# Kernel optimization log

Measured on AMD Instinct MI355X. Metric: run time of the kernel, lower is better.

## Reference

```python
import jax, jax.numpy as jnp
import numpy as np

NUM_NODES = 100000
NUM_HYPEREDGES = 100000
NNZ = 1600000
K = 64
LAMBDA_ORTHO = 0.1


def setup_inputs() -> dict:
    key = jax.random.key(0)
    k1, k2, k3 = jax.random.split(key, 3)
    Z = jax.random.normal(k1, (NUM_NODES, K), dtype=jnp.float32)
    hyperedge_index = jax.random.randint(k2, (2, NNZ), 0, NUM_HYPEREDGES, dtype=jnp.int64)
    hyperedge_weight = jax.random.uniform(k3, (NUM_HYPEREDGES,), dtype=jnp.float32)
    return {
        "Z": Z,
        "hyperedge_index": hyperedge_index,
        "num_nodes": NUM_NODES,
        "hyperedge_weight": hyperedge_weight,
    }


def reference(Z, hyperedge_index, num_nodes, hyperedge_weight):
    E = hyperedge_weight.shape[0]  # num_hyperedges (static)
    node_idx = hyperedge_index[0]
    edge_idx = hyperedge_index[1]

    # Node degree Dv = sum of incident hyperedge weights; clamp zeros to 1.
    w_exp = hyperedge_weight[edge_idx]                                  # [nnz]
    Dv = jax.ops.segment_sum(w_exp, node_idx, num_segments=num_nodes)   # [N]
    Dv = jnp.where(Dv == 0, jnp.ones_like(Dv), Dv)
    Y = Z * (Dv ** -0.5)[:, None]                                       # [N, k]

    # Hyperedge cardinality De (clamped) and raw counts n_e.
    ones = jnp.ones_like(edge_idx, dtype=Z.dtype)
    n_e = jax.ops.segment_sum(ones, edge_idx, num_segments=E)           # [E]
    De = jnp.where(n_e == 0, jnp.ones_like(n_e), n_e)

    # Closed form for the per-edge pairwise-distance loop:
    # 0.5 * sum_{i,j in e} |y_i - y_j|^2 = n_e * sum_i |y_i|^2 - |sum_i y_i|^2
    Yg = Y[node_idx]                                                    # [nnz, k]
    sum_e = jax.ops.segment_sum(Yg, edge_idx, num_segments=E)           # [E, k]
    ss_e = jax.ops.segment_sum(jnp.sum(Yg * Yg, axis=-1), edge_idx, num_segments=E)  # [E]
    per_edge = n_e * ss_e - jnp.sum(sum_e * sum_e, axis=-1)             # [E]
    loss = jnp.sum(hyperedge_weight / De * per_edge)

    # Orthogonality penalty: ||Y^T Y - I||_F
    k = Z.shape[1]
    G = Y.T @ Y - jnp.eye(k, dtype=Z.dtype)
    ortho_loss = jnp.sqrt(jnp.sum(G * G))

    return loss + LAMBDA_ORTHO * ortho_loss
```

## Files before the change

### kernel.cpp

```cpp
#include <hip/hip_runtime.h>
#include <math.h>

#define NNODES 100000
#define NEDGES 100000
#define NNZV   1600000
#define KDIM   64
#define LAMBDA 0.1f

#define NB    782
#define BSH   7
#define BMASK 127
#define CAP   3072
#define A0B   256
#define A0T   1024
#define CHUNK 6250
#define YQB   1024
#define GMB   512

#define OFF_DV      0
#define OFF_G       400128
#define OFF_PART    416512
#define OFF_ZN      419840
#define OFF_GC1     423936
#define OFF_GC2     427264
#define OFF_S1      430592
#define OFF_S2      10039808
#define OFF_YQ      19649024
#define OFF_GPART   26049024

#if defined(__has_builtin)
#if __has_builtin(__builtin_amdgcn_cvt_f32_fp8)
#define HAS_CVT_FP8 1
#endif
#if __has_builtin(__builtin_amdgcn_cvt_pk_fp8_f32)
#define HAS_PK_FP8 1
#endif
#endif

__device__ __forceinline__ int load_node(const unsigned* idx, int i, bool i64) {
    return (int)(i64 ? idx[2 * i] : idx[i]);
}
__device__ __forceinline__ int load_edge(const unsigned* idx, int i, bool i64) {
    return (int)(i64 ? idx[2 * (NNZV + i)] : idx[NNZV + i]);
}

__device__ __forceinline__ unsigned char enc_fp8(float x) {
    unsigned u = __float_as_uint(x);
    unsigned s = (u >> 31) << 7;
    unsigned mag = u & 0x7FFFFFFFu;
    if (mag >= 0x43E00000u) return (unsigned char)(s | 0x7Eu);
    if (mag < 0x3C800000u) {
        float a = __uint_as_float(mag);
        int m = (int)rintf(a * 512.0f);
        if (m >= 8) return (unsigned char)(s | 0x08u);
        return (unsigned char)(s | (unsigned)m);
    }
    unsigned lsb = (mag >> 20) & 1u;
    mag += 0x0007FFFFu + lsb;
    unsigned e = (mag >> 23) - 120u;
    return (unsigned char)(s | (e << 3) | ((mag >> 20) & 7u));
}

__device__ __forceinline__ unsigned pack_fp8x4(float y0, float y1, float y2, float y3) {
#ifdef HAS_PK_FP8
    int q = 0;
    q = __builtin_amdgcn_cvt_pk_fp8_f32(y0, y1, q, false);
    q = __builtin_amdgcn_cvt_pk_fp8_f32(y2, y3, q, true);
    return (unsigned)q;
#else
    return (unsigned)enc_fp8(y0) | ((unsigned)enc_fp8(y1) << 8) |
           ((unsigned)enc_fp8(y2) << 16) | ((unsigned)enc_fp8(y3) << 24);
#endif
}

template <int SEL>
__device__ __forceinline__ float dec_fp8(unsigned v) {
#ifdef HAS_CVT_FP8
    return __builtin_amdgcn_cvt_f32_fp8(v, SEL);
#else
    unsigned b = (v >> (8 * SEL)) & 0xFFu;
    unsigned e = (b >> 3) & 15u, m = b & 7u;
    float f = e ? __uint_as_float(((e + 120u) << 23) | (m << 20))
                : (float)m * 0.001953125f;
    return (b & 128u) ? -f : f;
#endif
}

__global__ void init_kernel(unsigned* __restrict__ gcur1, unsigned* __restrict__ gcur2) {
    int b = blockIdx.x * 256 + threadIdx.x;
    if (b < NB) {
        gcur1[b] = (unsigned)b * CAP;
        gcur2[b] = (unsigned)b * CAP;
    }
}

__global__ __launch_bounds__(A0T) void sort_kernel(const unsigned* __restrict__ idx,
                                                   unsigned* __restrict__ gcur1,
                                                   unsigned* __restrict__ gcur2,
                                                   unsigned* __restrict__ S1,
                                                   unsigned* __restrict__ S2) {
    __shared__ unsigned stage[CHUNK];
    __shared__ unsigned lhist[NB], lcur[NB], gbase[NB];
    __shared__ unsigned wsum[16], fred[16];
    int which = blockIdx.x >> 8, chunk = blockIdx.x & (A0B - 1);
    int t = threadIdx.x, wave = t >> 6, lane = t & 63;

    unsigned hv = idx[2 * t + 1];
#pragma unroll
    for (int off = 32; off; off >>= 1) hv |= __shfl_xor(hv, off);
    if (lane == 0) fred[wave] = hv;
    for (int j = t; j < NB; j += A0T) lhist[j] = 0u;
    __syncthreads();
    unsigned o = 0;
#pragma unroll
    for (int k = 0; k < 16; ++k) o |= fred[k];
    bool i64 = (o == 0u);

    int base = chunk * CHUNK;
    if (which == 0) {
        for (int i = base + t; i < base + CHUNK; i += A0T)
            atomicAdd(&lhist[load_edge(idx, i, i64) >> BSH], 1u);
    } else {
        for (int i = base + t; i < base + CHUNK; i += A0T)
            atomicAdd(&lhist[load_node(idx, i, i64) >> BSH], 1u);
    }
    __syncthreads();

    unsigned v = (t < NB) ? lhist[t] : 0u;
    unsigned x = v;
#pragma unroll
    for (int off = 1; off < 64; off <<= 1) {
        unsigned y = __shfl_up(x, off);
        if (lane >= off) x += y;
    }
    if (lane == 63) wsum[wave] = x;
    __syncthreads();
    if (t < 16) {
        unsigned a = wsum[t], y = a;
#pragma unroll
        for (int off = 1; off < 16; off <<= 1) {
            unsigned z = __shfl_up(y, off);
            if (t >= off) y += z;
        }
        wsum[t] = y - a;
    }
    __syncthreads();
    if (t < NB) lcur[t] = wsum[wave] + x - v;
    __syncthreads();

    for (int i = base + t; i < base + CHUNK; i += A0T) {
        int node = load_node(idx, i, i64);
        int edge = load_edge(idx, i, i64);
        unsigned key, val;
        if (which == 0) {
            key = (unsigned)edge >> BSH;
            val = (unsigned)node | ((unsigned)(edge & BMASK) << 17);
        } else {
            key = (unsigned)node >> BSH;
            val = (unsigned)edge | ((unsigned)(node & BMASK) << 17);
        }
        unsigned p = atomicAdd(&lcur[key], 1u);
        stage[p] = val;
    }
    __syncthreads();

    unsigned* gcur = which ? gcur2 : gcur1;
    if (t < NB) {
        unsigned c = lhist[t];
        gbase[t] = c ? atomicAdd(&gcur[t], c) : 0u;
    }
    __syncthreads();

    unsigned* S = which ? S2 : S1;
    int li = lane & 7;
    for (int bb = wave * 8 + (lane >> 3); bb < NB; bb += 128) {
        unsigned c = lhist[bb];
        unsigned st = lcur[bb] - c;
        unsigned g = gbase[bb];
        for (unsigned m = li; m < c; m += 8) S[g + m] = stage[st + m];
    }
}

__global__ __launch_bounds__(256) void dvb_kernel(const unsigned* __restrict__ S2,
                                                  const unsigned* __restrict__ gcur2,
                                                  const float* __restrict__ w,
                                                  float* __restrict__ Dv) {
    __shared__ float acc[128];
    int t = threadIdx.x, b = blockIdx.x;
    if (t < 128) acc[t] = 0.0f;
    __syncthreads();
    unsigned cnt = gcur2[b] - (unsigned)b * CAP;
    const unsigned* src = S2 + (size_t)b * CAP;
    for (unsigned i = t; i < cnt; i += 256) {
        unsigned e = src[i];
        atomicAdd(&acc[e >> 17], w[e & 0x1FFFFu]);
    }
    __syncthreads();
    int node = b * 128 + t;
    if (t < 128 && node < NNODES) Dv[node] = acc[t];
}

__global__ __launch_bounds__(256) void yq_kernel(const float* __restrict__ Z,
                                                 const float* __restrict__ Dv,
                                                 unsigned* __restrict__ Yq32,
                                                 float* __restrict__ ZN) {
    __shared__ float red[256];
    int t = threadIdx.x;
    float zn = 0.0f;
    for (int i4 = blockIdx.x * 256 + t; i4 < NNODES * 16; i4 += YQB * 256) {
        float4 v = ((const float4*)Z)[i4];
        float d = Dv[i4 >> 4];
        bool good = d > 0.0f;
        float r = good ? rsqrtf(d) : 1.0f;
        zn += good ? (v.x * v.x + v.y * v.y + v.z * v.z + v.w * v.w) : 0.0f;
        Yq32[i4] = pack_fp8x4(v.x * r, v.y * r, v.z * r, v.w * r);
    }
    red[t] = zn;
    __syncthreads();
    for (int s = 128; s > 0; s >>= 1) {
        if (t < s) red[t] += red[t + s];
        __syncthreads();
    }
    if (t == 0) ZN[blockIdx.x] = red[0];
}

__global__ __launch_bounds__(256) void gmat_kernel(const unsigned* __restrict__ Yq32,
                                                   float* __restrict__ Gpart) {
    __shared__ float ys[64][KDIM];
    float acc[16];
#pragma unroll
    for (int i = 0; i < 16; ++i) acc[i] = 0.0f;
    int t = threadIdx.x;
    int c = t & 63;
    int r0 = (t >> 6) * 16;
    for (int base = blockIdx.x * 64; base < NNODES; base += GMB * 64) {
        int rows = min(64, NNODES - base);
        __syncthreads();
        for (int j = t; j < rows * 16; j += 256) {
            unsigned v = Yq32[base * 16 + j];
            int row = j >> 4, q4 = (j & 15) * 4;
            ys[row][q4 + 0] = dec_fp8<0>(v);
            ys[row][q4 + 1] = dec_fp8<1>(v);
            ys[row][q4 + 2] = dec_fp8<2>(v);
            ys[row][q4 + 3] = dec_fp8<3>(v);
        }
        __syncthreads();
#pragma unroll 4
        for (int i = 0; i < rows; ++i) {
            float yc = ys[i][c];
#pragma unroll
            for (int rr = 0; rr < 16; ++rr) acc[rr] += ys[i][r0 + rr] * yc;
        }
    }
    float* gp = Gpart + (size_t)blockIdx.x * (KDIM * KDIM);
#pragma unroll
    for (int rr = 0; rr < 16; ++rr) gp[(r0 + rr) * KDIM + c] = acc[rr];
}

__global__ __launch_bounds__(256) void greduce_kernel(const float* __restrict__ Gpart,
                                                      float* __restrict__ G) {
    __shared__ float r[256];
    int t = threadIdx.x;
    int e0 = blockIdx.x * 32;
    int psub = t >> 5, e = e0 + (t & 31);
    float s = 0.0f;
    for (int p = psub; p < GMB; p += 8)
        s += Gpart[(size_t)p * (KDIM * KDIM) + e];
    r[t] = s;
    __syncthreads();
    if (t < 32) {
        float v = r[t];
#pragma unroll
        for (int k = 1; k < 8; ++k) v += r[t + 32 * k];
        G[e0 + t] = v;
    }
}

__global__ __launch_bounds__(512) void bedge_kernel(const unsigned* __restrict__ Yq32,
                                                    const float* __restrict__ w,
                                                    const unsigned* __restrict__ S1,
                                                    const unsigned* __restrict__ gcur1,
                                                    float* __restrict__ part) {
    __shared__ unsigned lhist[128], loffs[128], lcur[128];
    __shared__ unsigned snode[CAP];
    __shared__ float wred[8];
    int t = threadIdx.x, b = blockIdx.x;
    if (t < 128) lhist[t] = 0u;
    __syncthreads();
    unsigned cnt = gcur1[b] - (unsigned)b * CAP;
    const unsigned* src = S1 + (size_t)b * CAP;
    for (unsigned i = t; i < cnt; i += 512)
        atomicAdd(&lhist[src[i] >> 17], 1u);
    __syncthreads();
    if (t < 64) {
        unsigned a = lhist[2 * t], bb = lhist[2 * t + 1];
        unsigned sp = a + bb, x = sp;
#pragma unroll
        for (int off = 1; off < 64; off <<= 1) {
            unsigned y = __shfl_up(x, off);
            if (t >= off) x += y;
        }
        unsigned ex = x - sp;
        loffs[2 * t] = ex;          lcur[2 * t] = ex;
        loffs[2 * t + 1] = ex + a;  lcur[2 * t + 1] = ex + a;
    }
    __syncthreads();
    for (unsigned i = t; i < cnt; i += 512) {
        unsigned e = src[i];
        unsigned pos = atomicAdd(&lcur[e >> 17], 1u);
        snode[pos] = e & 0x1FFFFu;
    }
    __syncthreads();
    int wv = t >> 6, lane = t & 63, ms = lane >> 4, kq = lane & 15;
    float acc = 0.0f;
    for (int el = wv; el < 64; el += 8) {
        int eA = el, eB = el + 64;
        unsigned nA = lhist[eA], nB = lhist[eB];
        if (nA == 0 && nB == 0) continue;
        unsigned begA = loffs[eA], begB = loffs[eB];
        float a0 = 0, a1 = 0, a2 = 0, a3 = 0;
        float c0 = 0, c1 = 0, c2 = 0, c3 = 0;
        unsigned mmax = nA > nB ? nA : nB;
        for (unsigned m = 0; m < mmax; m += 16) {
            unsigned mA0 = m + (unsigned)ms, mA1 = mA0 + 4, mA2 = mA0 + 8, mA3 = mA0 + 12;
            bool oA0 = mA0 < nA, oA1 = mA1 < nA, oA2 = mA2 < nA, oA3 = mA3 < nA;
            bool oB0 = mA0 < nB, oB1 = mA1 < nB, oB2 = mA2 < nB, oB3 = mA3 < nB;
            unsigned nA0 = snode[oA0 ? begA + mA0 : 0];
            unsigned nA1 = snode[oA1 ? begA + mA1 : 0];
            unsigned nA2 = snode[oA2 ? begA + mA2 : 0];
            unsigned nA3 = snode[oA3 ? begA + mA3 : 0];
            unsigned nB0 = snode[oB0 ? begB + mA0 : 0];
            unsigned nB1 = snode[oB1 ? begB + mA1 : 0];
            unsigned nB2 = snode[oB2 ? begB + mA2 : 0];
            unsigned nB3 = snode[oB3 ? begB + mA3 : 0];
            unsigned vA0 = Yq32[nA0 * 16u + (unsigned)kq];
            unsigned vA1 = Yq32[nA1 * 16u + (unsigned)kq];
            unsigned vA2 = Yq32[nA2 * 16u + (unsigned)kq];
            unsigned vA3 = Yq32[nA3 * 16u + (unsigned)kq];
            unsigned vB0 = Yq32[nB0 * 16u + (unsigned)kq];
            unsigned vB1 = Yq32[nB1 * 16u + (unsigned)kq];
            unsigned vB2 = Yq32[nB2 * 16u + (unsigned)kq];
            unsigned vB3 = Yq32[nB3 * 16u + (unsigned)kq];
            if (oA0) { a0 += dec_fp8<0>(vA0); a1 += dec_fp8<1>(vA0);
                       a2 += dec_fp8<2>(vA0); a3 += dec_fp8<3>(vA0); }
            if (oA1) { a0 += dec_fp8<0>(vA1); a1 += dec_fp8<1>(vA1);
                       a2 += dec_fp8<2>(vA1); a3 += dec_fp8<3>(vA1); }
            if (oA2) { a0 += dec_fp8<0>(vA2); a1 += dec_fp8<1>(vA2);
                       a2 += dec_fp8<2>(vA2); a3 += dec_fp8<3>(vA2); }
            if (oA3) { a0 += dec_fp8<0>(vA3); a1 += dec_fp8<1>(vA3);
                       a2 += dec_fp8<2>(vA3); a3 += dec_fp8<3>(vA3); }
            if (oB0) { c0 += dec_fp8<0>(vB0); c1 += dec_fp8<1>(vB0);
                       c2 += dec_fp8<2>(vB0); c3 += dec_fp8<3>(vB0); }
            if (oB1) { c0 += dec_fp8<0>(vB1); c1 += dec_fp8<1>(vB1);
                       c2 += dec_fp8<2>(vB1); c3 += dec_fp8<3>(vB1); }
            if (oB2) { c0 += dec_fp8<0>(vB2); c1 += dec_fp8<1>(vB2);
                       c2 += dec_fp8<2>(vB2); c3 += dec_fp8<3>(vB2); }
            if (oB3) { c0 += dec_fp8<0>(vB3); c1 += dec_fp8<1>(vB3);
                       c2 += dec_fp8<2>(vB3); c3 += dec_fp8<3>(vB3); }
        }
        a0 += __shfl_xor(a0, 16); a0 += __shfl_xor(a0, 32);
        a1 += __shfl_xor(a1, 16); a1 += __shfl_xor(a1, 32);
        a2 += __shfl_xor(a2, 16); a2 += __shfl_xor(a2, 32);
        a3 += __shfl_xor(a3, 16); a3 += __shfl_xor(a3, 32);
        c0 += __shfl_xor(c0, 16); c0 += __shfl_xor(c0, 32);
        c1 += __shfl_xor(c1, 16); c1 += __shfl_xor(c1, 32);
        c2 += __shfl_xor(c2, 16); c2 += __shfl_xor(c2, 32);
        c3 += __shfl_xor(c3, 16); c3 += __shfl_xor(c3, 32);
        float aa = a0 * a0 + a1 * a1 + a2 * a2 + a3 * a3;
        float cc = c0 * c0 + c1 * c1 + c2 * c2 + c3 * c3;
        aa += __shfl_xor(aa, 1); aa += __shfl_xor(aa, 2);
        aa += __shfl_xor(aa, 4); aa += __shfl_xor(aa, 8);
        cc += __shfl_xor(cc, 1); cc += __shfl_xor(cc, 2);
        cc += __shfl_xor(cc, 4); cc += __shfl_xor(cc, 8);
        if (lane == 0) {
            if (nA) acc += (w[b * 128 + eA] / (float)nA) * aa;
            if (nB) acc += (w[b * 128 + eB] / (float)nB) * cc;
        }
    }
    if (lane == 0) wred[wv] = acc;
    __syncthreads();
    if (t == 0) {
        float s = 0.0f;
        for (int i = 0; i < 8; ++i) s += wred[i];
        part[b] = s;
    }
}

__global__ void final_kernel(const float* __restrict__ G,
                             const float* __restrict__ ZN,
                             const float* __restrict__ part,
                             float* __restrict__ out) {
    __shared__ float r1[256], r2[256];
    int t = threadIdx.x;
    float zn = 0.0f, pe = 0.0f, gg = 0.0f;
    for (int i = t; i < YQB; i += 256) zn += ZN[i];
    for (int i = t; i < NB; i += 256) pe += part[i];
    for (int i = t; i < KDIM * KDIM; i += 256) {
        int r = i >> 6, c = i & 63;
        float g = G[i] - ((r == c) ? 1.0f : 0.0f);
        gg += g * g;
    }
    r1[t] = zn - pe; r2[t] = gg;
    __syncthreads();
    for (int s = 128; s > 0; s >>= 1) {
        if (t < s) { r1[t] += r1[t + s]; r2[t] += r2[t + s]; }
        __syncthreads();
    }
    if (t == 0) out[0] = r1[0] + LAMBDA * sqrtf(r2[0]);
}

extern "C" void kernel_launch(void* const* d_in, const int* in_sizes, int n_in,
                              void* d_out, int out_size, void* d_ws, size_t ws_size,
                              hipStream_t stream) {
    const float* Z = (const float*)d_in[0];
    const unsigned* idx = (const unsigned*)d_in[1];
    const float* w = (const float*)d_in[3];
    float* out = (float*)d_out;
    char* ws = (char*)d_ws;

    float* Dv       = (float*)(ws + OFF_DV);
    float* G        = (float*)(ws + OFF_G);
    float* part     = (float*)(ws + OFF_PART);
    float* ZN       = (float*)(ws + OFF_ZN);
    unsigned* gcur1 = (unsigned*)(ws + OFF_GC1);
    unsigned* gcur2 = (unsigned*)(ws + OFF_GC2);
    unsigned* S1    = (unsigned*)(ws + OFF_S1);
    unsigned* S2    = (unsigned*)(ws + OFF_S2);
    unsigned* Yq32  = (unsigned*)(ws + OFF_YQ);
    float* Gpart    = (float*)(ws + OFF_GPART);

    init_kernel<<<4, 256, 0, stream>>>(gcur1, gcur2);
    sort_kernel<<<2 * A0B, A0T, 0, stream>>>(idx, gcur1, gcur2, S1, S2);
    dvb_kernel<<<NB, 256, 0, stream>>>(S2, gcur2, w, Dv);
    yq_kernel<<<YQB, 256, 0, stream>>>(Z, Dv, Yq32, ZN);
    bedge_kernel<<<NB, 512, 0, stream>>>(Yq32, w, S1, gcur1, part);
    gmat_kernel<<<GMB, 256, 0, stream>>>(Yq32, Gpart);
    greduce_kernel<<<128, 256, 0, stream>>>(Gpart, G);
    final_kernel<<<1, 256, 0, stream>>>(G, ZN, part, out);
}
```

Baseline: 130.4 us.

## Gather node rows with 16-byte loads and keep bucket entries in registers

The per-edge gather in bedge_kernel now loads each node's 64 fp8 features as four uint4 loads over 4 lanes, with 16 nodes in flight per wavefront, one edge per wave iteration. Previously it used 16 lanes per node with 32-bit loads and processed two edges at once. The bucket entries are also read once into six registers and reused for both the histogram and the scatter pass, which drops the second global read of S1. In exchange each lane holds 16 accumulators and the cross-lane reduction grows to 16 values per shuffle step. The register-held entries assume at most 6*512 entries per block, which matches CAP.

```diff
diff --git a/kernel.cpp b/kernel.cpp
--- a/kernel.cpp
+++ b/kernel.cpp
@@ -276,7 +276,7 @@
     }
 }
 
-__global__ __launch_bounds__(512) void bedge_kernel(const unsigned* __restrict__ Yq32,
+__global__ __launch_bounds__(512) void bedge_kernel(const uint4* __restrict__ Yq16,
                                                     const float* __restrict__ w,
                                                     const unsigned* __restrict__ S1,
                                                     const unsigned* __restrict__ gcur1,
@@ -289,8 +289,18 @@
     __syncthreads();
     unsigned cnt = gcur1[b] - (unsigned)b * CAP;
     const unsigned* src = S1 + (size_t)b * CAP;
-    for (unsigned i = t; i < cnt; i += 512)
-        atomicAdd(&lhist[src[i] >> 17], 1u);
+    unsigned e0 = (t + 0 * 512 < cnt) ? src[t + 0 * 512] : ~0u;
+    unsigned e1 = (t + 1 * 512 < cnt) ? src[t + 1 * 512] : ~0u;
+    unsigned e2 = (t + 2 * 512 < cnt) ? src[t + 2 * 512] : ~0u;
+    unsigned e3 = (t + 3 * 512 < cnt) ? src[t + 3 * 512] : ~0u;
+    unsigned e4 = (t + 4 * 512 < cnt) ? src[t + 4 * 512] : ~0u;
+    unsigned e5 = (t + 5 * 512 < cnt) ? src[t + 5 * 512] : ~0u;
+    if (e0 != ~0u) atomicAdd(&lhist[e0 >> 17], 1u);
+    if (e1 != ~0u) atomicAdd(&lhist[e1 >> 17], 1u);
+    if (e2 != ~0u) atomicAdd(&lhist[e2 >> 17], 1u);
+    if (e3 != ~0u) atomicAdd(&lhist[e3 >> 17], 1u);
+    if (e4 != ~0u) atomicAdd(&lhist[e4 >> 17], 1u);
+    if (e5 != ~0u) atomicAdd(&lhist[e5 >> 17], 1u);
     __syncthreads();
     if (t < 64) {
         unsigned a = lhist[2 * t], bb = lhist[2 * t + 1];
@@ -305,77 +315,48 @@
         loffs[2 * t + 1] = ex + a;  lcur[2 * t + 1] = ex + a;
     }
     __syncthreads();
-    for (unsigned i = t; i < cnt; i += 512) {
-        unsigned e = src[i];
-        unsigned pos = atomicAdd(&lcur[e >> 17], 1u);
-        snode[pos] = e & 0x1FFFFu;
-    }
-    __syncthreads();
-    int wv = t >> 6, lane = t & 63, ms = lane >> 4, kq = lane & 15;
+    if (e0 != ~0u) snode[atomicAdd(&lcur[e0 >> 17], 1u)] = e0 & 0x1FFFFu;
+    if (e1 != ~0u) snode[atomicAdd(&lcur[e1 >> 17], 1u)] = e1 & 0x1FFFFu;
+    if (e2 != ~0u) snode[atomicAdd(&lcur[e2 >> 17], 1u)] = e2 & 0x1FFFFu;
+    if (e3 != ~0u) snode[atomicAdd(&lcur[e3 >> 17], 1u)] = e3 & 0x1FFFFu;
+    if (e4 != ~0u) snode[atomicAdd(&lcur[e4 >> 17], 1u)] = e4 & 0x1FFFFu;
+    if (e5 != ~0u) snode[atomicAdd(&lcur[e5 >> 17], 1u)] = e5 & 0x1FFFFu;
+    __syncthreads();
+    int wv = t >> 6, lane = t & 63, ms = lane >> 2, q = lane & 3;
     float acc = 0.0f;
-    for (int el = wv; el < 64; el += 8) {
-        int eA = el, eB = el + 64;
-        unsigned nA = lhist[eA], nB = lhist[eB];
-        if (nA == 0 && nB == 0) continue;
-        unsigned begA = loffs[eA], begB = loffs[eB];
-        float a0 = 0, a1 = 0, a2 = 0, a3 = 0;
-        float c0 = 0, c1 = 0, c2 = 0, c3 = 0;
-        unsigned mmax = nA > nB ? nA : nB;
-        for (unsigned m = 0; m < mmax; m += 16) {
-            unsigned mA0 = m + (unsigned)ms, mA1 = mA0 + 4, mA2 = mA0 + 8, mA3 = mA0 + 12;
-            bool oA0 = mA0 < nA, oA1 = mA1 < nA, oA2 = mA2 < nA, oA3 = mA3 < nA;
-            bool oB0 = mA0 < nB, oB1 = mA1 < nB, oB2 = mA2 < nB, oB3 = mA3 < nB;
-            unsigned nA0 = snode[oA0 ? begA + mA0 : 0];
-            unsigned nA1 = snode[oA1 ? begA + mA1 : 0];
-            unsigned nA2 = snode[oA2 ? begA + mA2 : 0];
-            unsigned nA3 = snode[oA3 ? begA + mA3 : 0];
-            unsigned nB0 = snode[oB0 ? begB + mA0 : 0];
-            unsigned nB1 = snode[oB1 ? begB + mA1 : 0];
-            unsigned nB2 = snode[oB2 ? begB + mA2 : 0];
-            unsigned nB3 = snode[oB3 ? begB + mA3 : 0];
-            unsigned vA0 = Yq32[nA0 * 16u + (unsigned)kq];
-            unsigned vA1 = Yq32[nA1 * 16u + (unsigned)kq];
-            unsigned vA2 = Yq32[nA2 * 16u + (unsigned)kq];
-            unsigned vA3 = Yq32[nA3 * 16u + (unsigned)kq];
-            unsigned vB0 = Yq32[nB0 * 16u + (unsigned)kq];
-            unsigned vB1 = Yq32[nB1 * 16u + (unsigned)kq];
-            unsigned vB2 = Yq32[nB2 * 16u + (unsigned)kq];
-            unsigned vB3 = Yq32[nB3 * 16u + (unsigned)kq];
-            if (oA0) { a0 += dec_fp8<0>(vA0); a1 += dec_fp8<1>(vA0);
-                       a2 += dec_fp8<2>(vA0); a3 += dec_fp8<3>(vA0); }
-            if (oA1) { a0 += dec_fp8<0>(vA1); a1 += dec_fp8<1>(vA1);
-                       a2 += dec_fp8<2>(vA1); a3 += dec_fp8<3>(vA1); }
-            if (oA2) { a0 += dec_fp8<0>(vA2); a1 += dec_fp8<1>(vA2);
-                       a2 += dec_fp8<2>(vA2); a3 += dec_fp8<3>(vA2); }
-            if (oA3) { a0 += dec_fp8<0>(vA3); a1 += dec_fp8<1>(vA3);
-                       a2 += dec_fp8<2>(vA3); a3 += dec_fp8<3>(vA3); }
-            if (oB0) { c0 += dec_fp8<0>(vB0); c1 += dec_fp8<1>(vB0);
-                       c2 += dec_fp8<2>(vB0); c3 += dec_fp8<3>(vB0); }
-            if (oB1) { c0 += dec_fp8<0>(vB1); c1 += dec_fp8<1>(vB1);
-                       c2 += dec_fp8<2>(vB1); c3 += dec_fp8<3>(vB1); }
-            if (oB2) { c0 += dec_fp8<0>(vB2); c1 += dec_fp8<1>(vB2);
-                       c2 += dec_fp8<2>(vB2); c3 += dec_fp8<3>(vB2); }
-            if (oB3) { c0 += dec_fp8<0>(vB3); c1 += dec_fp8<1>(vB3);
-                       c2 += dec_fp8<2>(vB3); c3 += dec_fp8<3>(vB3); }
-        }
-        a0 += __shfl_xor(a0, 16); a0 += __shfl_xor(a0, 32);
-        a1 += __shfl_xor(a1, 16); a1 += __shfl_xor(a1, 32);
-        a2 += __shfl_xor(a2, 16); a2 += __shfl_xor(a2, 32);
-        a3 += __shfl_xor(a3, 16); a3 += __shfl_xor(a3, 32);
-        c0 += __shfl_xor(c0, 16); c0 += __shfl_xor(c0, 32);
-        c1 += __shfl_xor(c1, 16); c1 += __shfl_xor(c1, 32);
-        c2 += __shfl_xor(c2, 16); c2 += __shfl_xor(c2, 32);
-        c3 += __shfl_xor(c3, 16); c3 += __shfl_xor(c3, 32);
-        float aa = a0 * a0 + a1 * a1 + a2 * a2 + a3 * a3;
-        float cc = c0 * c0 + c1 * c1 + c2 * c2 + c3 * c3;
+    for (int el = wv; el < 128; el += 8) {
+        unsigned n = lhist[el];
+        if (!n) continue;
+        unsigned beg = loffs[el];
+        float s[16];
+#pragma unroll
+        for (int k = 0; k < 16; ++k) s[k] = 0.0f;
+        for (unsigned m = 0; m < n; m += 16) {
+            unsigned mi = m + (unsigned)ms;
+            bool ok = mi < n;
+            unsigned nd = snode[beg + (ok ? mi : 0)];
+            uint4 v = Yq16[nd * 4u + (unsigned)q];
+            if (ok) {
+                s[0] += dec_fp8<0>(v.x); s[1] += dec_fp8<1>(v.x);
+                s[2] += dec_fp8<2>(v.x); s[3] += dec_fp8<3>(v.x);
+                s[4] += dec_fp8<0>(v.y); s[5] += dec_fp8<1>(v.y);
+                s[6] += dec_fp8<2>(v.y); s[7] += dec_fp8<3>(v.y);
+                s[8] += dec_fp8<0>(v.z); s[9] += dec_fp8<1>(v.z);
+                s[10] += dec_fp8<2>(v.z); s[11] += dec_fp8<3>(v.z);
+                s[12] += dec_fp8<0>(v.w); s[13] += dec_fp8<1>(v.w);
+                s[14] += dec_fp8<2>(v.w); s[15] += dec_fp8<3>(v.w);
+            }
+        }
+#pragma unroll
+        for (int off = 4; off <= 32; off <<= 1) {
+#pragma unroll
+            for (int k = 0; k < 16; ++k) s[k] += __shfl_xor(s[k], off);
+        }
+        float aa = 0.0f;
+#pragma unroll
+        for (int k = 0; k < 16; ++k) aa += s[k] * s[k];
         aa += __shfl_xor(aa, 1); aa += __shfl_xor(aa, 2);
-        aa += __shfl_xor(aa, 4); aa += __shfl_xor(aa, 8);
-        cc += __shfl_xor(cc, 1); cc += __shfl_xor(cc, 2);
-        cc += __shfl_xor(cc, 4); cc += __shfl_xor(cc, 8);
-        if (lane == 0) {
-            if (nA) acc += (w[b * 128 + eA] / (float)nA) * aa;
-            if (nB) acc += (w[b * 128 + eB] / (float)nB) * cc;
-        }
+        if (lane == 0) acc += (w[b * 128 + el] / (float)n) * aa;
     }
     if (lane == 0) wred[wv] = acc;
     __syncthreads();
@@ -433,7 +414,7 @@
     sort_kernel<<<2 * A0B, A0T, 0, stream>>>(idx, gcur1, gcur2, S1, S2);
     dvb_kernel<<<NB, 256, 0, stream>>>(S2, gcur2, w, Dv);
     yq_kernel<<<YQB, 256, 0, stream>>>(Z, Dv, Yq32, ZN);
-    bedge_kernel<<<NB, 512, 0, stream>>>(Yq32, w, S1, gcur1, part);
+    bedge_kernel<<<NB, 512, 0, stream>>>((const uint4*)Yq32, w, S1, gcur1, part);
     gmat_kernel<<<GMB, 256, 0, stream>>>(Yq32, Gpart);
     greduce_kernel<<<128, 256, 0, stream>>>(Gpart, G);
     final_kernel<<<1, 256, 0, stream>>>(G, ZN, part, out);
```

Result: slower. 191.7 us (+47.1%).

## Fuse degree and FP8 quantization kernels, atomically reduce Gram, use packed FP8 decode

Applied to the files above, without the earlier changes.

Merges the node-degree bucket kernel with the Y quantization kernel, so each bucket block computes Dv in shared memory and immediately scales and packs its 128 nodes. This removes the Dv round trip through global memory and one launch. The Gram partial buffer and its reduce kernel are replaced by float atomicAdd into a zeroed G, which drops a launch and 8 MB of partial writes but adds atomic contention on 4096 addresses. FP8 decoding now uses the packed two-value convert builtin when it is available.

```diff
diff --git a/kernel.cpp b/kernel.cpp
--- a/kernel.cpp
+++ b/kernel.cpp
@@ -14,19 +14,16 @@
 #define A0B   256
 #define A0T   1024
 #define CHUNK 6250
-#define YQB   1024
 #define GMB   512
 
-#define OFF_DV      0
-#define OFF_G       400128
-#define OFF_PART    416512
-#define OFF_ZN      419840
-#define OFF_GC1     423936
-#define OFF_GC2     427264
-#define OFF_S1      430592
-#define OFF_S2      10039808
-#define OFF_YQ      19649024
-#define OFF_GPART   26049024
+#define OFF_G       0
+#define OFF_PART    16384
+#define OFF_ZN      19712
+#define OFF_GC1     23040
+#define OFF_GC2     26368
+#define OFF_S1      29696
+#define OFF_S2      9638912
+#define OFF_YQ      19248128
 
 #if defined(__has_builtin)
 #if __has_builtin(__builtin_amdgcn_cvt_f32_fp8)
@@ -34,6 +31,10 @@
 #endif
 #if __has_builtin(__builtin_amdgcn_cvt_pk_fp8_f32)
 #define HAS_PK_FP8 1
+#endif
+#if __has_builtin(__builtin_amdgcn_cvt_pk_f32_fp8)
+#define HAS_PK_F32_FP8 1
+typedef float f32x2 __attribute__((ext_vector_type(2)));
 #endif
 #endif
 
@@ -86,12 +87,27 @@
 #endif
 }
 
-__global__ void init_kernel(unsigned* __restrict__ gcur1, unsigned* __restrict__ gcur2) {
-    int b = blockIdx.x * 256 + threadIdx.x;
-    if (b < NB) {
-        gcur1[b] = (unsigned)b * CAP;
-        gcur2[b] = (unsigned)b * CAP;
-    }
+__device__ __forceinline__ void dec4_fp8(unsigned v, float& a0, float& a1,
+                                         float& a2, float& a3) {
+#ifdef HAS_PK_F32_FP8
+    f32x2 lo = __builtin_amdgcn_cvt_pk_f32_fp8((int)v, false);
+    f32x2 hi = __builtin_amdgcn_cvt_pk_f32_fp8((int)v, true);
+    a0 = lo.x; a1 = lo.y; a2 = hi.x; a3 = hi.y;
+#else
+    a0 = dec_fp8<0>(v); a1 = dec_fp8<1>(v);
+    a2 = dec_fp8<2>(v); a3 = dec_fp8<3>(v);
+#endif
+}
+
+__global__ void init_kernel(unsigned* __restrict__ gcur1,
+                            unsigned* __restrict__ gcur2,
+                            float* __restrict__ G) {
+    int i = blockIdx.x * 256 + threadIdx.x;
+    if (i < NB) {
+        gcur1[i] = (unsigned)i * CAP;
+        gcur2[i] = (unsigned)i * CAP;
+    }
+    if (i < KDIM * KDIM) G[i] = 0.0f;
 }
 
 __global__ __launch_bounds__(A0T) void sort_kernel(const unsigned* __restrict__ idx,
@@ -181,39 +197,37 @@
     }
 }
 
-__global__ __launch_bounds__(256) void dvb_kernel(const unsigned* __restrict__ S2,
-                                                  const unsigned* __restrict__ gcur2,
-                                                  const float* __restrict__ w,
-                                                  float* __restrict__ Dv) {
-    __shared__ float acc[128];
+__global__ __launch_bounds__(256) void dvyq_kernel(const unsigned* __restrict__ S2,
+                                                   const unsigned* __restrict__ gcur2,
+                                                   const float* __restrict__ w,
+                                                   const float* __restrict__ Z,
+                                                   unsigned* __restrict__ Yq32,
+                                                   float* __restrict__ ZN) {
+    __shared__ float accd[128];
+    __shared__ float red[256];
     int t = threadIdx.x, b = blockIdx.x;
-    if (t < 128) acc[t] = 0.0f;
+    if (t < 128) accd[t] = 0.0f;
     __syncthreads();
     unsigned cnt = gcur2[b] - (unsigned)b * CAP;
     const unsigned* src = S2 + (size_t)b * CAP;
     for (unsigned i = t; i < cnt; i += 256) {
         unsigned e = src[i];
-        atomicAdd(&acc[e >> 17], w[e & 0x1FFFFu]);
-    }
-    __syncthreads();
-    int node = b * 128 + t;
-    if (t < 128 && node < NNODES) Dv[node] = acc[t];
-}
-
-__global__ __launch_bounds__(256) void yq_kernel(const float* __restrict__ Z,
-                                                 const float* __restrict__ Dv,
-                                                 unsigned* __restrict__ Yq32,
-                                                 float* __restrict__ ZN) {
-    __shared__ float red[256];
-    int t = threadIdx.x;
+        atomicAdd(&accd[e >> 17], w[e & 0x1FFFFu]);
+    }
+    __syncthreads();
+    int base = b * 128;
     float zn = 0.0f;
-    for (int i4 = blockIdx.x * 256 + t; i4 < NNODES * 16; i4 += YQB * 256) {
-        float4 v = ((const float4*)Z)[i4];
-        float d = Dv[i4 >> 4];
-        bool good = d > 0.0f;
-        float r = good ? rsqrtf(d) : 1.0f;
-        zn += good ? (v.x * v.x + v.y * v.y + v.z * v.z + v.w * v.w) : 0.0f;
-        Yq32[i4] = pack_fp8x4(v.x * r, v.y * r, v.z * r, v.w * r);
+    for (int j = t; j < 128 * 16; j += 256) {
+        int row = j >> 4, q = j & 15;
+        int node = base + row;
+        if (node < NNODES) {
+            float4 v = ((const float4*)Z)[node * 16 + q];
+            float d = accd[row];
+            bool good = d > 0.0f;
+            float r = good ? rsqrtf(d) : 1.0f;
+            zn += good ? (v.x * v.x + v.y * v.y + v.z * v.z + v.w * v.w) : 0.0f;
+            Yq32[node * 16 + q] = pack_fp8x4(v.x * r, v.y * r, v.z * r, v.w * r);
+        }
     }
     red[t] = zn;
     __syncthreads();
@@ -221,11 +235,11 @@
         if (t < s) red[t] += red[t + s];
         __syncthreads();
     }
-    if (t == 0) ZN[blockIdx.x] = red[0];
+    if (t == 0) ZN[b] = red[0];
 }
 
 __global__ __launch_bounds__(256) void gmat_kernel(const unsigned* __restrict__ Yq32,
-                                                   float* __restrict__ Gpart) {
+                                                   float* __restrict__ G) {
     __shared__ float ys[64][KDIM];
     float acc[16];
 #pragma unroll
@@ -239,10 +253,12 @@
         for (int j = t; j < rows * 16; j += 256) {
             unsigned v = Yq32[base * 16 + j];
             int row = j >> 4, q4 = (j & 15) * 4;
-            ys[row][q4 + 0] = dec_fp8<0>(v);
-            ys[row][q4 + 1] = dec_fp8<1>(v);
-            ys[row][q4 + 2] = dec_fp8<2>(v);
-            ys[row][q4 + 3] = dec_fp8<3>(v);
+            float x0, x1, x2, x3;
+            dec4_fp8(v, x0, x1, x2, x3);
+            ys[row][q4 + 0] = x0;
+            ys[row][q4 + 1] = x1;
+            ys[row][q4 + 2] = x2;
+            ys[row][q4 + 3] = x3;
         }
         __syncthreads();
 #pragma unroll 4
@@ -252,28 +268,8 @@
             for (int rr = 0; rr < 16; ++rr) acc[rr] += ys[i][r0 + rr] * yc;
         }
     }
-    float* gp = Gpart + (size_t)blockIdx.x * (KDIM * KDIM);
-#pragma unroll
-    for (int rr = 0; rr < 16; ++rr) gp[(r0 + rr) * KDIM + c] = acc[rr];
-}
-
-__global__ __launch_bounds__(256) void greduce_kernel(const float* __restrict__ Gpart,
-                                                      float* __restrict__ G) {
-    __shared__ float r[256];
-    int t = threadIdx.x;
-    int e0 = blockIdx.x * 32;
-    int psub = t >> 5, e = e0 + (t & 31);
-    float s = 0.0f;
-    for (int p = psub; p < GMB; p += 8)
-        s += Gpart[(size_t)p * (KDIM * KDIM) + e];
-    r[t] = s;
-    __syncthreads();
-    if (t < 32) {
-        float v = r[t];
-#pragma unroll
-        for (int k = 1; k < 8; ++k) v += r[t + 32 * k];
-        G[e0 + t] = v;
-    }
+#pragma unroll
+    for (int rr = 0; rr < 16; ++rr) atomicAdd(&G[(r0 + rr) * KDIM + c], acc[rr]);
 }
 
 __global__ __launch_bounds__(512) void bedge_kernel(const unsigned* __restrict__ Yq32,
@@ -341,22 +337,23 @@
             unsigned vB1 = Yq32[nB1 * 16u + (unsigned)kq];
             unsigned vB2 = Yq32[nB2 * 16u + (unsigned)kq];
             unsigned vB3 = Yq32[nB3 * 16u + (unsigned)kq];
-            if (oA0) { a0 += dec_fp8<0>(vA0); a1 += dec_fp8<1>(vA0);
-                       a2 += dec_fp8<2>(vA0); a3 += dec_fp8<3>(vA0); }
-            if (oA1) { a0 += dec_fp8<0>(vA1); a1 += dec_fp8<1>(vA1);
-                       a2 += dec_fp8<2>(vA1); a3 += dec_fp8<3>(vA1); }
-            if (oA2) { a0 += dec_fp8<0>(vA2); a1 += dec_fp8<1>(vA2);
-                       a2 += dec_fp8<2>(vA2); a3 += dec_fp8<3>(vA2); }
-            if (oA3) { a0 += dec_fp8<0>(vA3); a1 += dec_fp8<1>(vA3);
-                       a2 += dec_fp8<2>(vA3); a3 += dec_fp8<3>(vA3); }
-            if (oB0) { c0 += dec_fp8<0>(vB0); c1 += dec_fp8<1>(vB0);
-                       c2 += dec_fp8<2>(vB0); c3 += dec_fp8<3>(vB0); }
-            if (oB1) { c0 += dec_fp8<0>(vB1); c1 += dec_fp8<1>(vB1);
-                       c2 += dec_fp8<2>(vB1); c3 += dec_fp8<3>(vB1); }
-            if (oB2) { c0 += dec_fp8<0>(vB2); c1 += dec_fp8<1>(vB2);
-                       c2 += dec_fp8<2>(vB2); c3 += dec_fp8<3>(vB2); }
-            if (oB3) { c0 += dec_fp8<0>(vB3); c1 += dec_fp8<1>(vB3);
-                       c2 += dec_fp8<2>(vB3); c3 += dec_fp8<3>(vB3); }
+            float x0, x1, x2, x3;
+            dec4_fp8(vA0, x0, x1, x2, x3);
+            if (oA0) { a0 += x0; a1 += x1; a2 += x2; a3 += x3; }
+            dec4_fp8(vA1, x0, x1, x2, x3);
+            if (oA1) { a0 += x0; a1 += x1; a2 += x2; a3 += x3; }
+            dec4_fp8(vA2, x0, x1, x2, x3);
+            if (oA2) { a0 += x0; a1 += x1; a2 += x2; a3 += x3; }
+            dec4_fp8(vA3, x0, x1, x2, x3);
+            if (oA3) { a0 += x0; a1 += x1; a2 += x2; a3 += x3; }
+            dec4_fp8(vB0, x0, x1, x2, x3);
+            if (oB0) { c0 += x0; c1 += x1; c2 += x2; c3 += x3; }
+            dec4_fp8(vB1, x0, x1, x2, x3);
+            if (oB1) { c0 += x0; c1 += x1; c2 += x2; c3 += x3; }
+            dec4_fp8(vB2, x0, x1, x2, x3);
+            if (oB2) { c0 += x0; c1 += x1; c2 += x2; c3 += x3; }
+            dec4_fp8(vB3, x0, x1, x2, x3);
+            if (oB3) { c0 += x0; c1 += x1; c2 += x2; c3 += x3; }
         }
         a0 += __shfl_xor(a0, 16); a0 += __shfl_xor(a0, 32);
         a1 += __shfl_xor(a1, 16); a1 += __shfl_xor(a1, 32);
@@ -393,8 +390,7 @@
     __shared__ float r1[256], r2[256];
     int t = threadIdx.x;
     float zn = 0.0f, pe = 0.0f, gg = 0.0f;
-    for (int i = t; i < YQB; i += 256) zn += ZN[i];
-    for (int i = t; i < NB; i += 256) pe += part[i];
+    for (int i = t; i < NB; i += 256) { zn += ZN[i]; pe += part[i]; }
     for (int i = t; i < KDIM * KDIM; i += 256) {
         int r = i >> 6, c = i & 63;
         float g = G[i] - ((r == c) ? 1.0f : 0.0f);
@@ -418,7 +414,6 @@
     float* out = (float*)d_out;
     char* ws = (char*)d_ws;
 
-    float* Dv       = (float*)(ws + OFF_DV);
     float* G        = (float*)(ws + OFF_G);
     float* part     = (float*)(ws + OFF_PART);
     float* ZN       = (float*)(ws + OFF_ZN);
@@ -427,14 +422,11 @@
     unsigned* S1    = (unsigned*)(ws + OFF_S1);
     unsigned* S2    = (unsigned*)(ws + OFF_S2);
     unsigned* Yq32  = (unsigned*)(ws + OFF_YQ);
-    float* Gpart    = (float*)(ws + OFF_GPART);
-
-    init_kernel<<<4, 256, 0, stream>>>(gcur1, gcur2);
+
+    init_kernel<<<16, 256, 0, stream>>>(gcur1, gcur2, G);
     sort_kernel<<<2 * A0B, A0T, 0, stream>>>(idx, gcur1, gcur2, S1, S2);
-    dvb_kernel<<<NB, 256, 0, stream>>>(S2, gcur2, w, Dv);
-    yq_kernel<<<YQB, 256, 0, stream>>>(Z, Dv, Yq32, ZN);
+    dvyq_kernel<<<NB, 256, 0, stream>>>(S2, gcur2, w, Z, Yq32, ZN);
     bedge_kernel<<<NB, 512, 0, stream>>>(Yq32, w, S1, gcur1, part);
-    gmat_kernel<<<GMB, 256, 0, stream>>>(Yq32, Gpart);
-    greduce_kernel<<<128, 256, 0, stream>>>(Gpart, G);
+    gmat_kernel<<<GMB, 256, 0, stream>>>(Yq32, G);
     final_kernel<<<1, 256, 0, stream>>>(G, ZN, part, out);
 }
```

Result: faster. 118.2 us (-9.4%).
